# Optimization experiments

Hardware: AMD Instinct MI355X
Metric: run time of the kernel (lower is better)

The kernel has to match this reference:

```python
import jax, jax.numpy as jnp
import numpy as np

CODEBOOK_SIZE = 8192
D_MODEL = 256
COMMITMENT_COST = 0.25


def setup_inputs() -> dict:
    key = jax.random.key(0)
    k1, k2 = jax.random.split(key)
    z = jax.random.normal(k1, (16, 512, D_MODEL), dtype=jnp.float32)
    # uniform(-1/K, 1/K) init like the torch module
    codebook = jax.random.uniform(
        k2, (CODEBOOK_SIZE, D_MODEL), dtype=jnp.float32,
        minval=-1.0 / CODEBOOK_SIZE, maxval=1.0 / CODEBOOK_SIZE)
    return {"z": z, "codebook": codebook}


def reference(z, codebook):
    B, P, D = z.shape
    flat = z.reshape(-1, D)  # [N, D]
    distances = (jnp.sum(flat * flat, axis=1, keepdims=True)
                 + jnp.sum(codebook * codebook, axis=1)
                 - 2.0 * jnp.matmul(flat, codebook.T))
    indices = jnp.argmin(distances, axis=1)  # [N] int
    quantized = codebook[indices]            # [N, D] gather
    # non-EMA VQ loss: codebook loss + commitment loss
    e_latent_loss = jnp.mean((jax.lax.stop_gradient(quantized) - flat) ** 2)
    q_latent_loss = jnp.mean((quantized - jax.lax.stop_gradient(flat)) ** 2)
    loss = q_latent_loss + COMMITMENT_COST * e_latent_loss
    # straight-through estimator
    quantized_st = flat + jax.lax.stop_gradient(quantized - flat)
    return (loss, quantized_st.reshape(B, P, D), indices.reshape(B, P))
```

## Files before the change

### kernel.cpp

```cpp
#include <hip/hip_runtime.h>
#include <hip/hip_bf16.h>
#include <math.h>


#define NROWS 8192
#define DDIM  256
#define KCW   8192
#define CAP   128
#define MARGIN 5e-4f

typedef __attribute__((ext_vector_type(8))) short short8;
typedef __attribute__((ext_vector_type(4))) float f32x4;

struct AFrag { short8 v[8]; f32x4 e2; };

__device__ inline unsigned fmap(float f) {
  unsigned b = __float_as_uint(f);
  return (b & 0x80000000u) ? ~b : (b | 0x80000000u);
}
__device__ inline float funmap(unsigned u) {
  unsigned b = (u & 0x80000000u) ? (u & 0x7FFFFFFFu) : ~u;
  return __uint_as_float(b);
}

__global__ __launch_bounds__(256) void k_prep_cast(const float* __restrict__ z,
                                                   const float* __restrict__ cb,
                                                   ushort* __restrict__ zb,
                                                   ushort* __restrict__ cbb,
                                                   float* __restrict__ e2f,
                                                   unsigned* __restrict__ rowMinU,
                                                   unsigned* __restrict__ cnt) {
  int t = threadIdx.x, w = t >> 6, lane = t & 63;
  int wid = blockIdx.x * 4 + w;
  bool isCb = wid >= NROWS;
  int row = isCb ? wid - NROWS : wid;
  const float* src = (isCb ? cb : z) + (size_t)row * DDIM + lane * 4;
  float4 v = *reinterpret_cast<const float4*>(src);
  ushort4 o;
  __hip_bfloat16 bx = __float2bfloat16(v.x); o.x = *(ushort*)&bx;
  __hip_bfloat16 by = __float2bfloat16(v.y); o.y = *(ushort*)&by;
  __hip_bfloat16 bz = __float2bfloat16(v.z); o.z = *(ushort*)&bz;
  __hip_bfloat16 bw = __float2bfloat16(v.w); o.w = *(ushort*)&bw;
  ushort* dst = (isCb ? cbb : zb) + (size_t)row * DDIM + lane * 4;
  *reinterpret_cast<ushort4*>(dst) = o;
  if (isCb) {
    double d = (double)v.x * v.x + (double)v.y * v.y + (double)v.z * v.z + (double)v.w * v.w;
#pragma unroll
    for (int off = 1; off < 64; off <<= 1) d += __shfl_xor(d, off);
    if (lane == 0) e2f[row] = (float)d;
  } else {
    if (lane == 0) { rowMinU[row] = ~0u; cnt[row] = 0; }
  }
}

__global__ __launch_bounds__(256, 2) void k_sweep(const ushort* __restrict__ zb,
                                                  const ushort* __restrict__ cbb,
                                                  const float* __restrict__ e2f,
                                                  unsigned* __restrict__ rowMinU,
                                                  unsigned* __restrict__ cnt,
                                                  ushort* __restrict__ cand) {
  int t = threadIdx.x, w = t >> 6, lane = t & 63;
  int wid = blockIdx.x * 4 + w;
  int rg = wid >> 4, sg = wid & 15;
  int R0 = rg * 64, C0 = sg * 512;
  int cl = lane & 15, g = lane >> 4;

  short8 Z[4][8];
#pragma unroll
  for (int n = 0; n < 4; ++n)
#pragma unroll
    for (int kk = 0; kk < 8; ++kk)
      Z[n][kk] = *reinterpret_cast<const short8*>(
          &zb[(size_t)(R0 + n * 16 + cl) * DDIM + kk * 32 + g * 8]);

  int rowIdx[4];
#pragma unroll
  for (int n = 0; n < 4; ++n) rowIdx[n] = R0 + n * 16 + cl;

  float runm[4] = {INFINITY, INFINITY, INFINITY, INFINITY};

  auto LOADA = [&](AFrag& A, int tile) {
    int CT = C0 + tile * 16;
#pragma unroll
    for (int kk = 0; kk < 8; ++kk)
      A.v[kk] = *reinterpret_cast<const short8*>(
          &cbb[(size_t)(CT + cl) * DDIM + kk * 32 + g * 8]);
    A.e2 = *reinterpret_cast<const f32x4*>(&e2f[CT + g * 4]);
  };

  auto COMPUTE = [&](const AFrag& A, int tile) {
    int CT = C0 + tile * 16;
    f32x4 acc[4];
#pragma unroll
    for (int n = 0; n < 4; ++n) acc[n] = (f32x4){0.f, 0.f, 0.f, 0.f};
#pragma unroll
    for (int kk = 0; kk < 8; ++kk)
#pragma unroll
      for (int n = 0; n < 4; ++n)
        acc[n] = __builtin_amdgcn_mfma_f32_16x16x32_bf16(A.v[kk], Z[n][kk], acc[n], 0, 0, 0);

#pragma unroll
    for (int n = 0; n < 4; ++n) {
      float s0 = __fsub_rn(A.e2[0], __fmul_rn(2.0f, acc[n][0]));
      float s1 = __fsub_rn(A.e2[1], __fmul_rn(2.0f, acc[n][1]));
      float s2 = __fsub_rn(A.e2[2], __fmul_rn(2.0f, acc[n][2]));
      float s3 = __fsub_rn(A.e2[3], __fmul_rn(2.0f, acc[n][3]));
      float jm = fminf(fminf(s0, s1), fminf(s2, s3));
      jm = fminf(jm, __shfl_xor(jm, 16));
      jm = fminf(jm, __shfl_xor(jm, 32));
      runm[n] = fminf(runm[n], jm);
      float thr = runm[n] + MARGIN;
      int row = rowIdx[n];
      int colb = CT + g * 4;
      if (s0 <= thr) { unsigned sl = atomicAdd(&cnt[row], 1u); if (sl < CAP) cand[(size_t)row * CAP + sl] = (ushort)(colb + 0); }
      if (s1 <= thr) { unsigned sl = atomicAdd(&cnt[row], 1u); if (sl < CAP) cand[(size_t)row * CAP + sl] = (ushort)(colb + 1); }
      if (s2 <= thr) { unsigned sl = atomicAdd(&cnt[row], 1u); if (sl < CAP) cand[(size_t)row * CAP + sl] = (ushort)(colb + 2); }
      if (s3 <= thr) { unsigned sl = atomicAdd(&cnt[row], 1u); if (sl < CAP) cand[(size_t)row * CAP + sl] = (ushort)(colb + 3); }
    }

    if (tile < 2 || (tile & 7) == 7) {
#pragma unroll
      for (int n = 0; n < 4; ++n) {
        if (g == n) atomicMin(&rowMinU[rowIdx[n]], fmap(runm[n]));
      }
#pragma unroll
      for (int n = 0; n < 4; ++n)
        runm[n] = fminf(runm[n], funmap(rowMinU[rowIdx[n]]));
    }
  };

  AFrag A0, A1;
  LOADA(A0, 0);
  for (int tile = 0; tile < 32; tile += 2) {
    if (tile + 1 < 32) LOADA(A1, tile + 1);
    COMPUTE(A0, tile);
    if (tile + 2 < 32) LOADA(A0, tile + 2);
    COMPUTE(A1, tile + 1);
  }
}

__global__ __launch_bounds__(256) void k_rescore_gather(const float* __restrict__ z,
                                                        const float* __restrict__ cb,
                                                        const float* __restrict__ e2f,
                                                        const unsigned* __restrict__ cnt,
                                                        const ushort* __restrict__ cand,
                                                        float* __restrict__ out_q,
                                                        float* __restrict__ out_idx,
                                                        float* __restrict__ lpart) {
  int t = threadIdx.x, w = t >> 6, lane = t & 63;
  int row = blockIdx.x * 4 + w;
  const float* xp = z + (size_t)row * DDIM;
  const float4* xp4 = reinterpret_cast<const float4*>(xp);
  float4 x4 = xp4[lane];
  double rd = (double)x4.x * x4.x + (double)x4.y * x4.y + (double)x4.z * x4.z + (double)x4.w * x4.w;
#pragma unroll
  for (int off = 1; off < 64; off <<= 1) rd += __shfl_xor(rd, off);
  float r2v = (float)rd;

  unsigned n = cnt[row];
  float s = INFINITY; int ci = 0x7fffffff;
  if (n <= CAP) {
#pragma unroll
    for (int base = 0; base < CAP; base += 64) {
      int k_i = base + lane;
      if (k_i < (int)n) {
        int c = cand[(size_t)row * CAP + k_i];
        const float4* ep4 = reinterpret_cast<const float4*>(cb + (size_t)c * DDIM);
        float acc = 0.f;
#pragma unroll 4
        for (int k4 = 0; k4 < 64; ++k4) {
          float4 e = ep4[k4], x = xp4[k4];
          acc = __fmaf_rn(x.x, e.x, acc);
          acc = __fmaf_rn(x.y, e.y, acc);
          acc = __fmaf_rn(x.z, e.z, acc);
          acc = __fmaf_rn(x.w, e.w, acc);
        }
        float scv = __fsub_rn(__fadd_rn(r2v, e2f[c]), __fmul_rn(2.0f, acc));
        if (scv < s || (scv == s && c < ci)) { s = scv; ci = c; }
      }
    }
  } else {
    for (int base = 0; base < KCW; base += 64) {
      int c = base + lane;
      const float4* ep4 = reinterpret_cast<const float4*>(cb + (size_t)c * DDIM);
      float acc = 0.f;
#pragma unroll 4
      for (int k4 = 0; k4 < 64; ++k4) {
        float4 e = ep4[k4], x = xp4[k4];
        acc = __fmaf_rn(x.x, e.x, acc);
        acc = __fmaf_rn(x.y, e.y, acc);
        acc = __fmaf_rn(x.z, e.z, acc);
        acc = __fmaf_rn(x.w, e.w, acc);
      }
      float scv = __fsub_rn(__fadd_rn(r2v, e2f[c]), __fmul_rn(2.0f, acc));
      if (scv < s) { s = scv; ci = c; }
    }
  }
#pragma unroll
  for (int off = 1; off < 64; off <<= 1) {
    float os = __shfl_xor(s, off); int oi = __shfl_xor(ci, off);
    if (os < s || (os == s && oi < ci)) { s = os; ci = oi; }
  }
  if (lane == 0) out_idx[row] = (float)ci;

  float4 qv = *reinterpret_cast<const float4*>(cb + (size_t)ci * DDIM + lane * 4);
  float* o = out_q + (size_t)row * DDIM + lane * 4;
  o[0] = qv.x; o[1] = qv.y; o[2] = qv.z; o[3] = qv.w;
  float dx = qv.x - x4.x, dy = qv.y - x4.y, dz = qv.z - x4.z, dw = qv.w - x4.w;
  double d = (double)dx * dx + (double)dy * dy + (double)dz * dz + (double)dw * dw;
#pragma unroll
  for (int off = 1; off < 64; off <<= 1) d += __shfl_xor(d, off);
  if (lane == 0) lpart[row] = (float)d;
}

__global__ __launch_bounds__(256) void k_loss(const float* __restrict__ lpart,
                                              float* __restrict__ out0) {
  __shared__ double red[256];
  int t = threadIdx.x;
  double s = 0.0;
  for (int j = t; j < NROWS; j += 256) s += lpart[j];
  red[t] = s;
  __syncthreads();
  for (int off = 128; off > 0; off >>= 1) {
    if (t < off) red[t] += red[t + off];
    __syncthreads();
  }
  if (t == 0) out0[0] = (float)(1.25 * red[0] / (double)((size_t)NROWS * DDIM));
}

extern "C" void kernel_launch(void* const* d_in, const int* in_sizes, int n_in,
                              void* d_out, int out_size, void* d_ws, size_t ws_size,
                              hipStream_t stream) {
  const float* z  = (const float*)d_in[0];
  const float* cb = (const float*)d_in[1];
  float* out = (float*)d_out;
  char* ws = (char*)d_ws;
  const size_t HALF = (size_t)NROWS * DDIM;

  ushort* zb  = (ushort*)(out + 4);
  ushort* cbb = zb + HALF;

  size_t off = 0;
  float*    e2f     = (float*)(ws + off);    off += NROWS * 4;
  unsigned* cnt     = (unsigned*)(ws + off); off += NROWS * 4;
  unsigned* rowMinU = (unsigned*)(ws + off);
  float*    lpart   = (float*)(ws + off);    off += NROWS * 4;
  ushort*   cand    = (ushort*)(ws + off);   off += (size_t)NROWS * CAP * 2;

  float* out_q   = out + 1;
  float* out_idx = out + 1 + HALF;

  k_prep_cast     <<<(2 * NROWS) / 4, 256, 0, stream>>>(z, cb, zb, cbb, e2f, rowMinU, cnt);
  k_sweep         <<<512,             256, 0, stream>>>(zb, cbb, e2f, rowMinU, cnt, cand);
  k_rescore_gather<<<NROWS / 4,       256, 0, stream>>>(z, cb, e2f, cnt, cand, out_q, out_idx, lpart);
  k_loss          <<<1,               256, 0, stream>>>(lpart, out);
}
```

Baseline: 207.9 us.

## Halve per-wave row tile in sweep, drop double buffering, raise occupancy

The sweep kernel now gives each wave 32 rows instead of 64, keeping only two Z fragments in registers. It also removes the manual double-buffered codebook fragment loads, and launches twice as many blocks with a minimum of 4 blocks per CU. The aim is to cut register pressure so more waves run at once and hide memory latency. In exchange, each codebook tile loaded from global memory is reused across half as many rows, which doubles codebook traffic, and the explicit prefetch overlap is lost.

```diff
diff --git a/kernel.cpp b/kernel.cpp
--- a/kernel.cpp
+++ b/kernel.cpp
@@ -11,8 +11,6 @@
 
 typedef __attribute__((ext_vector_type(8))) short short8;
 typedef __attribute__((ext_vector_type(4))) float f32x4;
-
-struct AFrag { short8 v[8]; f32x4 e2; };
 
 __device__ inline unsigned fmap(float f) {
   unsigned b = __float_as_uint(f);
@@ -53,7 +51,7 @@
   }
 }
 
-__global__ __launch_bounds__(256, 2) void k_sweep(const ushort* __restrict__ zb,
+__global__ __launch_bounds__(256, 4) void k_sweep(const ushort* __restrict__ zb,
                                                   const ushort* __restrict__ cbb,
                                                   const float* __restrict__ e2f,
                                                   unsigned* __restrict__ rowMinU,
@@ -62,80 +60,75 @@
   int t = threadIdx.x, w = t >> 6, lane = t & 63;
   int wid = blockIdx.x * 4 + w;
   int rg = wid >> 4, sg = wid & 15;
-  int R0 = rg * 64, C0 = sg * 512;
+  int R0 = rg * 32, C0 = sg * 512;
   int cl = lane & 15, g = lane >> 4;
 
-  short8 Z[4][8];
-#pragma unroll
-  for (int n = 0; n < 4; ++n)
+  short8 Z[2][8];
+#pragma unroll
+  for (int n = 0; n < 2; ++n)
 #pragma unroll
     for (int kk = 0; kk < 8; ++kk)
       Z[n][kk] = *reinterpret_cast<const short8*>(
           &zb[(size_t)(R0 + n * 16 + cl) * DDIM + kk * 32 + g * 8]);
 
-  int rowIdx[4];
-#pragma unroll
-  for (int n = 0; n < 4; ++n) rowIdx[n] = R0 + n * 16 + cl;
-
-  float runm[4] = {INFINITY, INFINITY, INFINITY, INFINITY};
-
-  auto LOADA = [&](AFrag& A, int tile) {
+  int row0 = R0 + cl, row1 = R0 + 16 + cl;
+  float runm0 = INFINITY, runm1 = INFINITY;
+
+  for (int tile = 0; tile < 32; ++tile) {
     int CT = C0 + tile * 16;
+    short8 A[8];
 #pragma unroll
     for (int kk = 0; kk < 8; ++kk)
-      A.v[kk] = *reinterpret_cast<const short8*>(
+      A[kk] = *reinterpret_cast<const short8*>(
           &cbb[(size_t)(CT + cl) * DDIM + kk * 32 + g * 8]);
-    A.e2 = *reinterpret_cast<const f32x4*>(&e2f[CT + g * 4]);
-  };
-
-  auto COMPUTE = [&](const AFrag& A, int tile) {
-    int CT = C0 + tile * 16;
-    f32x4 acc[4];
-#pragma unroll
-    for (int n = 0; n < 4; ++n) acc[n] = (f32x4){0.f, 0.f, 0.f, 0.f};
-#pragma unroll
-    for (int kk = 0; kk < 8; ++kk)
-#pragma unroll
-      for (int n = 0; n < 4; ++n)
-        acc[n] = __builtin_amdgcn_mfma_f32_16x16x32_bf16(A.v[kk], Z[n][kk], acc[n], 0, 0, 0);
-
-#pragma unroll
-    for (int n = 0; n < 4; ++n) {
-      float s0 = __fsub_rn(A.e2[0], __fmul_rn(2.0f, acc[n][0]));
-      float s1 = __fsub_rn(A.e2[1], __fmul_rn(2.0f, acc[n][1]));
-      float s2 = __fsub_rn(A.e2[2], __fmul_rn(2.0f, acc[n][2]));
-      float s3 = __fsub_rn(A.e2[3], __fmul_rn(2.0f, acc[n][3]));
+    f32x4 e2v = *reinterpret_cast<const f32x4*>(&e2f[CT + g * 4]);
+
+    f32x4 acc0 = (f32x4){0.f, 0.f, 0.f, 0.f};
+    f32x4 acc1 = (f32x4){0.f, 0.f, 0.f, 0.f};
+#pragma unroll
+    for (int kk = 0; kk < 8; ++kk) {
+      acc0 = __builtin_amdgcn_mfma_f32_16x16x32_bf16(A[kk], Z[0][kk], acc0, 0, 0, 0);
+      acc1 = __builtin_amdgcn_mfma_f32_16x16x32_bf16(A[kk], Z[1][kk], acc1, 0, 0, 0);
+    }
+
+    int colb = CT + g * 4;
+    {
+      float s0 = __fsub_rn(e2v[0], __fmul_rn(2.0f, acc0[0]));
+      float s1 = __fsub_rn(e2v[1], __fmul_rn(2.0f, acc0[1]));
+      float s2 = __fsub_rn(e2v[2], __fmul_rn(2.0f, acc0[2]));
+      float s3 = __fsub_rn(e2v[3], __fmul_rn(2.0f, acc0[3]));
       float jm = fminf(fminf(s0, s1), fminf(s2, s3));
       jm = fminf(jm, __shfl_xor(jm, 16));
       jm = fminf(jm, __shfl_xor(jm, 32));
-      runm[n] = fminf(runm[n], jm);
-      float thr = runm[n] + MARGIN;
-      int row = rowIdx[n];
-      int colb = CT + g * 4;
-      if (s0 <= thr) { unsigned sl = atomicAdd(&cnt[row], 1u); if (sl < CAP) cand[(size_t)row * CAP + sl] = (ushort)(colb + 0); }
-      if (s1 <= thr) { unsigned sl = atomicAdd(&cnt[row], 1u); if (sl < CAP) cand[(size_t)row * CAP + sl] = (ushort)(colb + 1); }
-      if (s2 <= thr) { unsigned sl = atomicAdd(&cnt[row], 1u); if (sl < CAP) cand[(size_t)row * CAP + sl] = (ushort)(colb + 2); }
-      if (s3 <= thr) { unsigned sl = atomicAdd(&cnt[row], 1u); if (sl < CAP) cand[(size_t)row * CAP + sl] = (ushort)(colb + 3); }
+      runm0 = fminf(runm0, jm);
+      float thr = runm0 + MARGIN;
+      if (s0 <= thr) { unsigned sl = atomicAdd(&cnt[row0], 1u); if (sl < CAP) cand[(size_t)row0 * CAP + sl] = (ushort)(colb + 0); }
+      if (s1 <= thr) { unsigned sl = atomicAdd(&cnt[row0], 1u); if (sl < CAP) cand[(size_t)row0 * CAP + sl] = (ushort)(colb + 1); }
+      if (s2 <= thr) { unsigned sl = atomicAdd(&cnt[row0], 1u); if (sl < CAP) cand[(size_t)row0 * CAP + sl] = (ushort)(colb + 2); }
+      if (s3 <= thr) { unsigned sl = atomicAdd(&cnt[row0], 1u); if (sl < CAP) cand[(size_t)row0 * CAP + sl] = (ushort)(colb + 3); }
+    }
+    {
+      float s0 = __fsub_rn(e2v[0], __fmul_rn(2.0f, acc1[0]));
+      float s1 = __fsub_rn(e2v[1], __fmul_rn(2.0f, acc1[1]));
+      float s2 = __fsub_rn(e2v[2], __fmul_rn(2.0f, acc1[2]));
+      float s3 = __fsub_rn(e2v[3], __fmul_rn(2.0f, acc1[3]));
+      float jm = fminf(fminf(s0, s1), fminf(s2, s3));
+      jm = fminf(jm, __shfl_xor(jm, 16));
+      jm = fminf(jm, __shfl_xor(jm, 32));
+      runm1 = fminf(runm1, jm);
+      float thr = runm1 + MARGIN;
+      if (s0 <= thr) { unsigned sl = atomicAdd(&cnt[row1], 1u); if (sl < CAP) cand[(size_t)row1 * CAP + sl] = (ushort)(colb + 0); }
+      if (s1 <= thr) { unsigned sl = atomicAdd(&cnt[row1], 1u); if (sl < CAP) cand[(size_t)row1 * CAP + sl] = (ushort)(colb + 1); }
+      if (s2 <= thr) { unsigned sl = atomicAdd(&cnt[row1], 1u); if (sl < CAP) cand[(size_t)row1 * CAP + sl] = (ushort)(colb + 2); }
+      if (s3 <= thr) { unsigned sl = atomicAdd(&cnt[row1], 1u); if (sl < CAP) cand[(size_t)row1 * CAP + sl] = (ushort)(colb + 3); }
     }
 
     if (tile < 2 || (tile & 7) == 7) {
-#pragma unroll
-      for (int n = 0; n < 4; ++n) {
-        if (g == n) atomicMin(&rowMinU[rowIdx[n]], fmap(runm[n]));
-      }
-#pragma unroll
-      for (int n = 0; n < 4; ++n)
-        runm[n] = fminf(runm[n], funmap(rowMinU[rowIdx[n]]));
-    }
-  };
-
-  AFrag A0, A1;
-  LOADA(A0, 0);
-  for (int tile = 0; tile < 32; tile += 2) {
-    if (tile + 1 < 32) LOADA(A1, tile + 1);
-    COMPUTE(A0, tile);
-    if (tile + 2 < 32) LOADA(A0, tile + 2);
-    COMPUTE(A1, tile + 1);
+      if (g == 0) atomicMin(&rowMinU[row0], fmap(runm0));
+      if (g == 1) atomicMin(&rowMinU[row1], fmap(runm1));
+      runm0 = fminf(runm0, funmap(rowMinU[row0]));
+      runm1 = fminf(runm1, funmap(rowMinU[row1]));
+    }
   }
 }
 
@@ -251,7 +244,7 @@
   float* out_idx = out + 1 + HALF;
 
   k_prep_cast     <<<(2 * NROWS) / 4, 256, 0, stream>>>(z, cb, zb, cbb, e2f, rowMinU, cnt);
-  k_sweep         <<<512,             256, 0, stream>>>(zb, cbb, e2f, rowMinU, cnt, cand);
+  k_sweep         <<<1024,            256, 0, stream>>>(zb, cbb, e2f, rowMinU, cnt, cand);
   k_rescore_gather<<<NROWS / 4,       256, 0, stream>>>(z, cb, e2f, cnt, cand, out_q, out_idx, lpart);
   k_loss          <<<1,               256, 0, stream>>>(lpart, out);
 }
```

After: 254.4 us. 22.4% more time.
